# Optimization experiments

Hardware: AMD Instinct MI355X
Metric: run time of the kernel (lower is better)

The kernel has to match this reference:

```python
import jax, jax.numpy as jnp
import numpy as np

B, D = 500000, 128
UNITS, STACK, NPRED = 4, 12, 2
EPS = 1e-3  # Keras BatchNormalization default epsilon


def setup_inputs() -> dict:
    key = jax.random.key(0)
    ks = jax.random.split(key, 2 * STACK + 4)
    inp = {"x": jax.random.normal(ks[0], (B, D), dtype=jnp.float32)}
    # 12 dense weights with growing input width D + 4*i
    for i in range(STACK):
        inp[f"w{i}"] = jax.random.normal(ks[1 + i], (D + UNITS * i, UNITS), dtype=jnp.float32) * 0.1
    inp["gamma"] = 1.0 + 0.1 * jax.random.normal(ks[STACK + 1], (STACK, UNITS), dtype=jnp.float32)
    inp["beta"] = 0.1 * jax.random.normal(ks[STACK + 2], (STACK, UNITS), dtype=jnp.float32)
    inp["mean"] = 0.1 * jax.random.normal(ks[STACK + 3], (STACK, UNITS), dtype=jnp.float32)
    inp["var"] = 0.5 + jax.random.uniform(ks[2 * STACK], (STACK, UNITS), dtype=jnp.float32)
    inp["wf"] = jax.random.normal(ks[2 * STACK + 1], (D + UNITS * STACK, NPRED), dtype=jnp.float32) * 0.1
    inp["bf"] = jnp.zeros((NPRED,), dtype=jnp.float32)
    return inp


def reference(x, w0, w1, w2, w3, w4, w5, w6, w7, w8, w9, w10, w11,
              gamma, beta, mean, var, wf, bf):
    ws = [w0, w1, w2, w3, w4, w5, w6, w7, w8, w9, w10, w11]
    h = x
    for i in range(STACK):
        y = h @ ws[i]  # [B, 4]
        # inference-mode BatchNorm, fused scale/shift
        scale = gamma[i] * jax.lax.rsqrt(var[i] + EPS)
        y = jax.nn.relu(y * scale + (beta[i] - mean[i] * scale))
        h = jnp.concatenate([y, h], axis=-1)  # width grows by 4
    logits = h @ wf + bf  # [B, 2]
    return jax.nn.softmax(logits, axis=-1)
```

## Files before the change

### kernel.cpp

```cpp
#include <hip/hip_runtime.h>

#define NROWS 500000
#define DD 128
#define NSTACK 12
#define BNEPS 1e-3f
#define NCOL 50
#define WXSTRIDE 52

typedef float v2f __attribute__((ext_vector_type(2)));
typedef float v4f __attribute__((ext_vector_type(4)));

__global__ __launch_bounds__(256) void predict_kernel(
    const float* __restrict__ x,
    const float* __restrict__ w0,  const float* __restrict__ w1,
    const float* __restrict__ w2,  const float* __restrict__ w3,
    const float* __restrict__ w4,  const float* __restrict__ w5,
    const float* __restrict__ w6,  const float* __restrict__ w7,
    const float* __restrict__ w8,  const float* __restrict__ w9,
    const float* __restrict__ w10, const float* __restrict__ w11,
    const float* __restrict__ gamma_, const float* __restrict__ beta_,
    const float* __restrict__ mean_,  const float* __restrict__ var_,
    const float* __restrict__ wf,     const float* __restrict__ bf,
    float* __restrict__ out)
{
    __shared__ __align__(16) float WX[DD * WXSTRIDE];
    __shared__ __align__(16) float WH[1056];
    __shared__ __align__(16) float WFY[96];
    __shared__ float SC[48];
    __shared__ float SH[48];
    __shared__ float BF[2];

    const int tid = threadIdx.x;
    const float* ws[NSTACK] = {w0,w1,w2,w3,w4,w5,w6,w7,w8,w9,w10,w11};

    for (int idx = tid; idx < DD * NCOL; idx += 256) {
        const int k = idx / NCOL;
        const int c = idx - k * NCOL;
        float v;
        if (c < 48) {
            const int i = c >> 2, u = c & 3;
            v = ws[i][16 * i + 4 * k + u];
        } else {
            v = wf[96 + 2 * k + (c - 48)];
        }
        WX[k * WXSTRIDE + c] = v;
    }
#pragma unroll
    for (int i = 1; i < NSTACK; ++i) {
        const int off = 8 * i * (i - 1);
        for (int idx = tid; idx < 16 * i; idx += 256) WH[off + idx] = ws[i][idx];
    }
    for (int idx = tid; idx < 96; idx += 256) WFY[idx] = wf[idx];
    if (tid < 48) {
        const float sc = gamma_[tid] / sqrtf(var_[tid] + BNEPS);
        SC[tid] = sc;
        SH[tid] = beta_[tid] - mean_[tid] * sc;
    }
    if (tid < 2) BF[tid] = bf[tid];
    __syncthreads();

    const int row = blockIdx.x * blockDim.x + tid;
    if (row >= NROWS) return;

    v2f T[25];
#pragma unroll
    for (int j = 0; j < 25; ++j) T[j] = (v2f){0.0f, 0.0f};

    const v4f* __restrict__ xv = (const v4f*)(x + (size_t)row * DD);

#pragma unroll 2
    for (int kk = 0; kk < DD / 4; ++kk) {
        const v4f xc = xv[kk];
#pragma unroll
        for (int c = 0; c < 4; ++c) {
            const float xk = xc[c];
            const float* wrow = &WX[(kk * 4 + c) * WXSTRIDE];
#pragma unroll
            for (int j = 0; j < NSTACK; ++j) {
                const v4f w = *(const v4f*)(wrow + 4 * j);
                T[2 * j]     += xk * (v2f){w.x, w.y};
                T[2 * j + 1] += xk * (v2f){w.z, w.w};
            }
            const v2f w2 = *(const v2f*)(wrow + 48);
            T[24] += xk * w2;
        }
    }

    float y[NSTACK * 4];
#pragma unroll
    for (int i = 0; i < NSTACK; ++i) {
        float acc0 = T[2 * i].x, acc1 = T[2 * i].y;
        float acc2 = T[2 * i + 1].x, acc3 = T[2 * i + 1].y;
        const float* wh = &WH[8 * i * (i - 1)];
#pragma unroll
        for (int m = 0; m < 4 * i; ++m) {
            const float hv = y[(i - 1 - (m >> 2)) * 4 + (m & 3)];
            const v4f wv = *(const v4f*)(wh + 4 * m);
            acc0 += hv * wv.x; acc1 += hv * wv.y;
            acc2 += hv * wv.z; acc3 += hv * wv.w;
        }
        const float* sc = &SC[4 * i];
        const float* sh = &SH[4 * i];
        float r0 = acc0 * sc[0] + sh[0];
        float r1 = acc1 * sc[1] + sh[1];
        float r2 = acc2 * sc[2] + sh[2];
        float r3 = acc3 * sc[3] + sh[3];
        y[i * 4 + 0] = r0 > 0.0f ? r0 : 0.0f;
        y[i * 4 + 1] = r1 > 0.0f ? r1 : 0.0f;
        y[i * 4 + 2] = r2 > 0.0f ? r2 : 0.0f;
        y[i * 4 + 3] = r3 > 0.0f ? r3 : 0.0f;
    }

    float l0 = T[24].x + BF[0];
    float l1 = T[24].y + BF[1];
#pragma unroll
    for (int m = 0; m < 48; ++m) {
        const float hv = y[(11 - (m >> 2)) * 4 + (m & 3)];
        const v2f wv = *(const v2f*)(&WFY[2 * m]);
        l0 += hv * wv.x;
        l1 += hv * wv.y;
    }

    const float mx = fmaxf(l0, l1);
    const float e0 = __expf(l0 - mx);
    const float e1 = __expf(l1 - mx);
    const float inv = 1.0f / (e0 + e1);
    *(v2f*)(out + (size_t)row * 2) = (v2f){e0 * inv, e1 * inv};
}

extern "C" void kernel_launch(void* const* d_in, const int* in_sizes, int n_in,
                              void* d_out, int out_size, void* d_ws, size_t ws_size,
                              hipStream_t stream) {
    const float* x   = (const float*)d_in[0];
    const float* w0  = (const float*)d_in[1];
    const float* w1  = (const float*)d_in[2];
    const float* w2  = (const float*)d_in[3];
    const float* w3  = (const float*)d_in[4];
    const float* w4  = (const float*)d_in[5];
    const float* w5  = (const float*)d_in[6];
    const float* w6  = (const float*)d_in[7];
    const float* w7  = (const float*)d_in[8];
    const float* w8  = (const float*)d_in[9];
    const float* w9  = (const float*)d_in[10];
    const float* w10 = (const float*)d_in[11];
    const float* w11 = (const float*)d_in[12];
    const float* gm  = (const float*)d_in[13];
    const float* bt  = (const float*)d_in[14];
    const float* mn  = (const float*)d_in[15];
    const float* vr  = (const float*)d_in[16];
    const float* wf  = (const float*)d_in[17];
    const float* bf  = (const float*)d_in[18];
    float* out = (float*)d_out;

    dim3 block(256);
    dim3 grid((NROWS + 255) / 256);
    hipLaunchKernelGGL(predict_kernel, grid, block, 0, stream,
                       x, w0, w1, w2, w3, w4, w5, w6, w7, w8, w9, w10, w11,
                       gm, bt, mn, vr, wf, bf, out);
}
```

Before: 458.4 us.

## Process four rows per thread to reuse shared-memory weight loads

Each thread now computes four rows, so every LDS weight vector it reads feeds four rows' FMAs instead of one. This lowers LDS traffic per FLOP and amortises the block's weight staging over four times as many rows, with a grid a quarter the size. The cost is 200 accumulator registers per thread. A launch-bounds minimum of two blocks per CU caps VGPRs, which may cause spills. Occupancy also drops, which can hurt hiding of the strided per-row global x loads.

```diff
diff --git a/kernel.cpp b/kernel.cpp
--- a/kernel.cpp
+++ b/kernel.cpp
@@ -6,11 +6,12 @@
 #define BNEPS 1e-3f
 #define NCOL 50
 #define WXSTRIDE 52
+#define RPT 4
 
 typedef float v2f __attribute__((ext_vector_type(2)));
 typedef float v4f __attribute__((ext_vector_type(4)));
 
-__global__ __launch_bounds__(256) void predict_kernel(
+__global__ __launch_bounds__(256, 2) void predict_kernel(
     const float* __restrict__ x,
     const float* __restrict__ w0,  const float* __restrict__ w1,
     const float* __restrict__ w2,  const float* __restrict__ w3,
@@ -59,73 +60,95 @@
     if (tid < 2) BF[tid] = bf[tid];
     __syncthreads();
 
-    const int row = blockIdx.x * blockDim.x + tid;
-    if (row >= NROWS) return;
+    const int base = blockIdx.x * (256 * RPT) + tid;
+    int  rowc [RPT];
+    bool valid[RPT];
+#pragma unroll
+    for (int r = 0; r < RPT; ++r) {
+        const int rr = base + 256 * r;
+        valid[r] = rr < NROWS;
+        rowc[r]  = valid[r] ? rr : (NROWS - 1);
+    }
+    const v4f* __restrict__ xv[RPT];
+#pragma unroll
+    for (int r = 0; r < RPT; ++r) xv[r] = (const v4f*)(x + (size_t)rowc[r] * DD);
 
-    v2f T[25];
+    v2f T[RPT][25];
 #pragma unroll
-    for (int j = 0; j < 25; ++j) T[j] = (v2f){0.0f, 0.0f};
+    for (int r = 0; r < RPT; ++r)
+#pragma unroll
+        for (int j = 0; j < 25; ++j) T[r][j] = (v2f){0.0f, 0.0f};
 
-    const v4f* __restrict__ xv = (const v4f*)(x + (size_t)row * DD);
-
-#pragma unroll 2
     for (int kk = 0; kk < DD / 4; ++kk) {
-        const v4f xc = xv[kk];
+        v4f xc[RPT];
+#pragma unroll
+        for (int r = 0; r < RPT; ++r) xc[r] = xv[r][kk];
 #pragma unroll
         for (int c = 0; c < 4; ++c) {
-            const float xk = xc[c];
             const float* wrow = &WX[(kk * 4 + c) * WXSTRIDE];
 #pragma unroll
             for (int j = 0; j < NSTACK; ++j) {
                 const v4f w = *(const v4f*)(wrow + 4 * j);
-                T[2 * j]     += xk * (v2f){w.x, w.y};
-                T[2 * j + 1] += xk * (v2f){w.z, w.w};
+                const v2f wlo = {w.x, w.y};
+                const v2f whi = {w.z, w.w};
+#pragma unroll
+                for (int r = 0; r < RPT; ++r) {
+                    const float xk = xc[r][c];
+                    T[r][2 * j]     += xk * wlo;
+                    T[r][2 * j + 1] += xk * whi;
+                }
             }
             const v2f w2 = *(const v2f*)(wrow + 48);
-            T[24] += xk * w2;
+#pragma unroll
+            for (int r = 0; r < RPT; ++r) T[r][24] += xc[r][c] * w2;
         }
     }
 
-    float y[NSTACK * 4];
 #pragma unroll
-    for (int i = 0; i < NSTACK; ++i) {
-        float acc0 = T[2 * i].x, acc1 = T[2 * i].y;
-        float acc2 = T[2 * i + 1].x, acc3 = T[2 * i + 1].y;
-        const float* wh = &WH[8 * i * (i - 1)];
+    for (int r = 0; r < RPT; ++r) {
+        float y[NSTACK * 4];
 #pragma unroll
-        for (int m = 0; m < 4 * i; ++m) {
-            const float hv = y[(i - 1 - (m >> 2)) * 4 + (m & 3)];
-            const v4f wv = *(const v4f*)(wh + 4 * m);
-            acc0 += hv * wv.x; acc1 += hv * wv.y;
-            acc2 += hv * wv.z; acc3 += hv * wv.w;
+        for (int i = 0; i < NSTACK; ++i) {
+            float acc0 = T[r][2 * i].x, acc1 = T[r][2 * i].y;
+            float acc2 = T[r][2 * i + 1].x, acc3 = T[r][2 * i + 1].y;
+            const float* wh = &WH[8 * i * (i - 1)];
+#pragma unroll
+            for (int m = 0; m < 4 * i; ++m) {
+                const float hv = y[(i - 1 - (m >> 2)) * 4 + (m & 3)];
+                const v4f wv = *(const v4f*)(wh + 4 * m);
+                acc0 += hv * wv.x; acc1 += hv * wv.y;
+                acc2 += hv * wv.z; acc3 += hv * wv.w;
+            }
+            const float* sc = &SC[4 * i];
+            const float* sh = &SH[4 * i];
+            float r0 = acc0 * sc[0] + sh[0];
+            float r1 = acc1 * sc[1] + sh[1];
+            float r2 = acc2 * sc[2] + sh[2];
+            float r3 = acc3 * sc[3] + sh[3];
+            y[i * 4 + 0] = r0 > 0.0f ? r0 : 0.0f;
+            y[i * 4 + 1] = r1 > 0.0f ? r1 : 0.0f;
+            y[i * 4 + 2] = r2 > 0.0f ? r2 : 0.0f;
+            y[i * 4 + 3] = r3 > 0.0f ? r3 : 0.0f;
         }
-        const float* sc = &SC[4 * i];
-        const float* sh = &SH[4 * i];
-        float r0 = acc0 * sc[0] + sh[0];
-        float r1 = acc1 * sc[1] + sh[1];
-        float r2 = acc2 * sc[2] + sh[2];
-        float r3 = acc3 * sc[3] + sh[3];
-        y[i * 4 + 0] = r0 > 0.0f ? r0 : 0.0f;
-        y[i * 4 + 1] = r1 > 0.0f ? r1 : 0.0f;
-        y[i * 4 + 2] = r2 > 0.0f ? r2 : 0.0f;
-        y[i * 4 + 3] = r3 > 0.0f ? r3 : 0.0f;
+
+        float l0 = T[r][24].x + BF[0];
+        float l1 = T[r][24].y + BF[1];
+#pragma unroll
+        for (int m = 0; m < 48; ++m) {
+            const float hv = y[(11 - (m >> 2)) * 4 + (m & 3)];
+            const v2f wv = *(const v2f*)(&WFY[2 * m]);
+            l0 += hv * wv.x;
+            l1 += hv * wv.y;
+        }
+
+        const float mx = fmaxf(l0, l1);
+        const float e0 = __expf(l0 - mx);
+        const float e1 = __expf(l1 - mx);
+        const float inv = 1.0f / (e0 + e1);
+        if (valid[r]) {
+            *(v2f*)(out + (size_t)rowc[r] * 2) = (v2f){e0 * inv, e1 * inv};
+        }
     }
-
-    float l0 = T[24].x + BF[0];
-    float l1 = T[24].y + BF[1];
-#pragma unroll
-    for (int m = 0; m < 48; ++m) {
-        const float hv = y[(11 - (m >> 2)) * 4 + (m & 3)];
-        const v2f wv = *(const v2f*)(&WFY[2 * m]);
-        l0 += hv * wv.x;
-        l1 += hv * wv.y;
-    }
-
-    const float mx = fmaxf(l0, l1);
-    const float e0 = __expf(l0 - mx);
-    const float e1 = __expf(l1 - mx);
-    const float inv = 1.0f / (e0 + e1);
-    *(v2f*)(out + (size_t)row * 2) = (v2f){e0 * inv, e1 * inv};
 }
 
 extern "C" void kernel_launch(void* const* d_in, const int* in_sizes, int n_in,
@@ -152,8 +175,9 @@
     const float* bf  = (const float*)d_in[18];
     float* out = (float*)d_out;
 
+    const int rows_per_block = 256 * RPT;
     dim3 block(256);
-    dim3 grid((NROWS + 255) / 256);
+    dim3 grid((NROWS + rows_per_block - 1) / rows_per_block);
     hipLaunchKernelGGL(predict_kernel, grid, block, 0, stream,
                        x, w0, w1, w2, w3, w4, w5, w6, w7, w8, w9, w10, w11,
                        gm, bt, mn, vr, wf, bf, out);
```

New measurement: 1.036 ms. 126% more time.
